# Optimization experiments

Hardware: AMD Instinct MI355X
Metric: run time of the kernel (lower is better)

## Reference

```python
import jax, jax.numpy as jnp
import numpy as np

PH, PW = 7, 7          # pooled_height, pooled_width
SCALE = 0.0625         # spatial_scale
K = 6                  # static max integer cells per bin side (max bin size = 448*SCALE/7 = 4)


def setup_inputs() -> dict:
    key = jax.random.key(0)
    kf, kb, kx, ky, kw, kh = jax.random.split(key, 6)
    B, C, H, W = 4, 256, 64, 64
    R = 1024
    features = jax.random.normal(kf, (B, C, H, W), dtype=jnp.float32)
    # rois rows: (batch_idx, x1, y1, x2, y2) in image coords (image ~1024px, scale 1/16)
    bidx = jax.random.randint(kb, (R,), 0, B).astype(jnp.float32)
    x1 = jax.random.uniform(kx, (R,), minval=0.0, maxval=576.0)
    y1 = jax.random.uniform(ky, (R,), minval=0.0, maxval=576.0)
    bw = jax.random.uniform(kw, (R,), minval=32.0, maxval=448.0)
    bh = jax.random.uniform(kh, (R,), minval=32.0, maxval=448.0)
    rois = jnp.stack([bidx, x1, y1, x1 + bw, y1 + bh], axis=1)
    return {"features": features, "rois": rois}


def _gather(features, b, hidx, widx, H, W):
    # hidx: [R,PH] int32, widx: [R,PW] int32 -> [R,PH,PW,C]; out-of-bounds reads are zero
    vh = (hidx >= 0) & (hidx < H)
    vw = (widx >= 0) & (widx < W)
    mask = (vh[:, :, None] & vw[:, None, :]).astype(features.dtype)  # [R,PH,PW]
    hc = jnp.clip(hidx, 0, H - 1)
    wc = jnp.clip(widx, 0, W - 1)
    d = features[b[:, None, None], :, hc[:, :, None], wc[:, None, :]]  # [R,PH,PW,C]
    return d * mask[..., None]


def _cell_weights(start, end, s):
    # exact integrals of the two 1D bilinear hat weights over [start,end] clipped to cell [s, s+1]
    y0 = jnp.maximum(start, s)
    yl = jnp.maximum(jnp.minimum(end, s + 1.0), y0)  # empty intersection -> zero weights
    a = y0 - s
    la = yl - s
    g0 = la - 0.5 * la * la - a + 0.5 * a * a  # weight of node at s
    g1 = 0.5 * la * la - 0.5 * a * a           # weight of node at s+1
    return g0, g1


def prroi_pool(features, rois):
    B, C, H, W = features.shape
    R = rois.shape[0]
    dt = features.dtype
    b = rois[:, 0].astype(jnp.int32)
    x1 = rois[:, 1] * SCALE
    y1 = rois[:, 2] * SCALE
    x2 = rois[:, 3] * SCALE
    y2 = rois[:, 4] * SCALE
    roi_w = jnp.maximum(x2 - x1, 0.0)
    roi_h = jnp.maximum(y2 - y1, 0.0)
    bin_w = roi_w / PW
    bin_h = roi_h / PH
    # per-bin continuous windows [ws, we)
    ws_w = x1[:, None] + bin_w[:, None] * jnp.arange(PW, dtype=dt)  # [R,PW]
    ws_h = y1[:, None] + bin_h[:, None] * jnp.arange(PH, dtype=dt)  # [R,PH]
    we_w = ws_w + bin_w[:, None]
    we_h = ws_h + bin_h[:, None]
    s0_w = jnp.floor(ws_w)
    s0_h = jnp.floor(ws_h)

    offs = np.stack(np.meshgrid(np.arange(K), np.arange(K), indexing="ij"), -1).reshape(-1, 2)
    offs = jnp.asarray(offs, dtype=dt)  # [K*K, 2] (dh, dw)

    def step(acc, off):
        sh = s0_h + off[0]  # [R,PH] float (integer-valued)
        sw = s0_w + off[1]  # [R,PW]
        gy0, gy1 = _cell_weights(ws_h, we_h, sh)
        gx0, gx1 = _cell_weights(ws_w, we_w, sw)
        hi = sh.astype(jnp.int32)
        wi = sw.astype(jnp.int32)
        d00 = _gather(features, b, hi, wi, H, W)
        d01 = _gather(features, b, hi, wi + 1, H, W)
        d10 = _gather(features, b, hi + 1, wi, H, W)
        d11 = _gather(features, b, hi + 1, wi + 1, H, W)
        gy0 = gy0[:, :, None, None]
        gy1 = gy1[:, :, None, None]
        gx0 = gx0[:, None, :, None]
        gx1 = gx1[:, None, :, None]
        contrib = d00 * (gy0 * gx0) + d01 * (gy0 * gx1) + d10 * (gy1 * gx0) + d11 * (gy1 * gx1)
        return acc + contrib, None

    acc0 = jnp.zeros((R, PH, PW, C), dtype=dt)
    acc, _ = jax.lax.scan(step, acc0, offs)
    win = (bin_w * bin_h)[:, None, None, None]  # bin area in feature coords
    out = jnp.where(win > 0, acc / jnp.where(win > 0, win, 1.0), 0.0)
    return jnp.transpose(out, (0, 3, 1, 2))  # [R, C, PH, PW]


def reference(features, rois):
    return prroi_pool(features, rois)
```

## Files before the change

### kernel.cpp

```cpp
#include <hip/hip_runtime.h>
#include <hip/hip_fp16.h>

#define R_    1024
#define B_    4
#define C_    256
#define H_    64
#define W_    64
#define HW_   4096
#define PHW_  49
#define ROIT  128
#define LROWF 258
#define SLACKH 16896

__device__ __forceinline__ void cell_w(float start, float end, float s, float& g0, float& g1) {
    float y0 = fmaxf(start, s);
    float yl = fmaxf(fminf(end, s + 1.0f), y0);
    float a  = y0 - s;
    float la = yl - s;
    g0 = la - 0.5f * la * la - a + 0.5f * a * a;
    g1 = 0.5f * la * la - 0.5f * a * a;
}

__device__ __forceinline__ float4 h4_to_f4(uint2 u) {
    __half2 a = *reinterpret_cast<__half2*>(&u.x);
    __half2 b = *reinterpret_cast<__half2*>(&u.y);
    float2 fa = __half22float2(a);
    float2 fb = __half22float2(b);
    return make_float4(fa.x, fa.y, fb.x, fb.y);
}

__global__ __launch_bounds__(256) void prep(const float* __restrict__ in,
                                            __half* __restrict__ fTh,
                                            const float* __restrict__ rois,
                                            int* __restrict__ perm,
                                            float* __restrict__ roitab) {
    int bid = blockIdx.x;
    if (bid < 4096) {
        __shared__ float tile[32][33];
        int b   = bid >> 10;
        int rem = bid & 1023;
        int c0  = (rem >> 7) * 32;
        int p0  = (rem & 127) * 32;
        int tx  = threadIdx.x & 31;
        int ty  = threadIdx.x >> 5;
        const float* src = in + (size_t)b * C_ * HW_;
#pragma unroll
        for (int i = 0; i < 32; i += 8)
            tile[ty + i][tx] = src[(size_t)(c0 + ty + i) * HW_ + (p0 + tx)];
        __syncthreads();
        __half2* dsth = (__half2*)(fTh + (size_t)b * HW_ * C_);
#pragma unroll
        for (int i = 0; i < 2; ++i) {
            int idx = threadIdx.x + i * 256;
            int py  = idx >> 4;
            int cp  = idx & 15;
            float lo = tile[cp * 2][py];
            float hi = tile[cp * 2 + 1][py];
            dsth[(size_t)(p0 + py) * (C_ / 2) + (c0 >> 1) + cp] = __floats2half2_rn(lo, hi);
        }
        return;
    }
    if (bid == 4096) {
        if (threadIdx.x >= 64) {
            for (int j = threadIdx.x - 64; j < SLACKH; j += 192)
                fTh[(size_t)B_ * HW_ * C_ + j] = __half(0.0f);
            return;
        }
        int lane = threadIdx.x;
        unsigned long long below = (1ull << lane) - 1ull;
        int key[16];
#pragma unroll
        for (int i = 0; i < 16; ++i) {
            int idx = i * 64 + lane;
            const float* roi = rois + idx * 5;
            int b = (int)roi[0];
            float yc = (roi[2] + roi[4]) * 0.5f * 0.0625f;
            int yb = min(3, max(0, (int)(yc * 0.0625f)));
            key[i] = b * 4 + yb;
        }
        int cntk[16];
#pragma unroll
        for (int k = 0; k < 16; ++k) cntk[k] = 0;
        for (int i = 0; i < 16; ++i)
#pragma unroll
            for (int k = 0; k < 16; ++k)
                cntk[k] += __popcll(__ballot(key[i] == k));
        int off[16]; int acc = 0;
#pragma unroll
        for (int k = 0; k < 16; ++k) { off[k] = acc; acc += cntk[k]; }
        for (int i = 0; i < 16; ++i) {
#pragma unroll
            for (int k = 0; k < 16; ++k) {
                unsigned long long m = __ballot(key[i] == k);
                if (key[i] == k)
                    perm[off[k] + __popcll(m & below)] = i * 64 + lane;
                off[k] += __popcll(m);
            }
        }
        return;
    }
    int i = (bid - 4097) * 256 + threadIdx.x;
    int r  = i / PHW_;
    int k  = i - r * PHW_;
    int ph = k / 7, pw = k - ph * 7;
    const float* roi = rois + r * 5;
    int bb = (int)roi[0];
    float x1 = roi[1] * 0.0625f, y1 = roi[2] * 0.0625f;
    float x2 = roi[3] * 0.0625f, y2 = roi[4] * 0.0625f;
    float rw = fmaxf(x2 - x1, 0.0f), rh = fmaxf(y2 - y1, 0.0f);
    float bw = rw / 7.0f, bh = rh / 7.0f;
    float win = bw * bh;
    float* rt = roitab + (size_t)r * ROIT;

    float wy[8], wx[7];
#pragma unroll
    for (int t = 0; t < 7; ++t) { wy[t] = 0.0f; wx[t] = 0.0f; }
    wy[7] = 0.0f;
    int w0 = 0, h0 = 0, npy = 0, w00 = 0;
    float invwin = 0.0f;
    if (win > 0.0f) {
        float ws = x1 + bw * (float)pw, we = ws + bw;
        float hs = y1 + bh * (float)ph, he = hs + bh;
        float s0w = floorf(ws), s0h = floorf(hs);
        w0 = (int)s0w; h0 = (int)s0h;
        w00 = (int)floorf(x1);
#pragma unroll
        for (int o = 0; o < 6; ++o) {
            float g0, g1;
            cell_w(hs, he, s0h + (float)o, g0, g1);
            wy[o] += g0; wy[o + 1] += g1;
            cell_w(ws, we, s0w + (float)o, g0, g1);
            wx[o] += g0; wx[o + 1] += g1;
        }
        npy = min(7, max(0, (int)ceilf(he - s0h + 1.0f)));
        int npx = min(7, max(0, (int)ceilf(we - s0w + 1.0f)));
        npy = max(0, min(npy, H_ - h0));
        npx = max(0, min(npx, W_ - w0));
#pragma unroll
        for (int t = 0; t < 7; ++t) {
            if (t >= npx) wx[t] = 0.0f;
            if (t >= npy) wy[t] = 0.0f;
        }
        invwin = 1.0f / win;
    }
    if (ph == 0) {
#pragma unroll
        for (int t = 0; t < 7; ++t) rt[pw * 7 + t] = wx[t];
        rt[49 + pw] = __int_as_float(w0 - w00);
    }
    if (pw == 0) {
#pragma unroll
        for (int t = 0; t < 8; ++t) rt[72 + ph * 8 + t] = wy[t] * invwin;
        rt[64 + ph] = __int_as_float(h0 | (npy << 8));
    }
    if (k == 0) {
        int jlim = 0;
        if (win > 0.0f) {
#pragma unroll
            for (int p = 0; p < 7; ++p) {
                float wsp = x1 + bw * (float)p, wep = wsp + bw;
                float s0wp = floorf(wsp);
                int w0p = (int)s0wp;
                int npxp = min(7, max(0, (int)ceilf(wep - s0wp + 1.0f)));
                npxp = max(0, min(npxp, W_ - w0p));
                jlim = max(jlim, (w0p - w00) + npxp);
            }
        }
        rt[63] = __int_as_float(bb | (w00 << 8) | (jlim << 16));
    }
}

__global__ __launch_bounds__(256) void prroi_rows(const __half* __restrict__ fTh,
                                                  const int* __restrict__ perm,
                                                  const float* __restrict__ roitab,
                                                  __half* __restrict__ scr) {
    __shared__ __align__(16) float colw[4][32 * 8];
    int wid  = __builtin_amdgcn_readfirstlane(threadIdx.x >> 6);
    int lane = threadIdx.x & 63;
    float* cwv = colw[wid];
    int bid = blockIdx.x;
    int g   = (bid & 7) * 896 + (bid >> 3) * 4 + wid;
    int rs  = g / 7;
    int ph  = g - rs * 7;
    int r   = __builtin_amdgcn_readfirstlane(perm[rs]);
    const float* rt = roitab + (size_t)r * ROIT;

#pragma unroll
    for (int u = 0; u < 4; ++u) cwv[lane + u * 64] = 0.0f;
    if (lane < 49) {
        int pw = lane / 7;
        int dx = lane - pw * 7;
        float wxv = rt[lane];
        int d = __float_as_int(rt[49 + pw]);
        cwv[(d + dx) * 8 + pw] = wxv;
    }
    int meta = __float_as_int(rt[63]);
    int bb   = meta & 0xff;
    int w00  = (meta >> 8) & 0xff;
    int jlim = (meta >> 16) & 0xff;
    int hm   = __float_as_int(rt[64 + ph]);
    int h0   = hm & 0xff;
    int npy  = (hm >> 8) & 0xff;
    int npy2 = (npy + 1) & ~1;
    const float* wyp = rt + 72 + ph * 8;
    const __half* fr = fTh + ((size_t)bb * HW_ + (size_t)h0 * W_ + w00) * C_ + lane * 4;

    float4 acc[7];
#pragma unroll
    for (int p = 0; p < 7; ++p) acc[p] = make_float4(0.f, 0.f, 0.f, 0.f);

    for (int jl = 0; jl < jlim; jl += 2) {
        const __half* cp = fr + (size_t)jl * C_;
        float4 gA = make_float4(0.f, 0.f, 0.f, 0.f);
        float4 gB = make_float4(0.f, 0.f, 0.f, 0.f);
        for (int dy = 0; dy < npy2; dy += 2) {
            const __half* r0 = cp + (size_t)dy * (W_ * C_);
            uint2 va0 = *(const uint2*)(r0);
            uint2 vb0 = *(const uint2*)(r0 + C_);
            uint2 va1 = *(const uint2*)(r0 + W_ * C_);
            uint2 vb1 = *(const uint2*)(r0 + W_ * C_ + C_);
            float w0y = wyp[dy];
            float w1y = wyp[dy + 1];
            float4 fa0 = h4_to_f4(va0);
            float4 fb0 = h4_to_f4(vb0);
            float4 fa1 = h4_to_f4(va1);
            float4 fb1 = h4_to_f4(vb1);
            gA.x = fmaf(w0y, fa0.x, fmaf(w1y, fa1.x, gA.x));
            gA.y = fmaf(w0y, fa0.y, fmaf(w1y, fa1.y, gA.y));
            gA.z = fmaf(w0y, fa0.z, fmaf(w1y, fa1.z, gA.z));
            gA.w = fmaf(w0y, fa0.w, fmaf(w1y, fa1.w, gA.w));
            gB.x = fmaf(w0y, fb0.x, fmaf(w1y, fb1.x, gB.x));
            gB.y = fmaf(w0y, fb0.y, fmaf(w1y, fb1.y, gB.y));
            gB.z = fmaf(w0y, fb0.z, fmaf(w1y, fb1.z, gB.z));
            gB.w = fmaf(w0y, fb0.w, fmaf(w1y, fb1.w, gB.w));
        }
        float4 ca0 = *(const float4*)(cwv + jl * 8);
        float4 ca1 = *(const float4*)(cwv + jl * 8 + 4);
        float4 cb0 = *(const float4*)(cwv + jl * 8 + 8);
        float4 cb1 = *(const float4*)(cwv + jl * 8 + 12);
#define ACCP(P, CA, CB) { \
    acc[P].x = fmaf(CA, gA.x, fmaf(CB, gB.x, acc[P].x)); \
    acc[P].y = fmaf(CA, gA.y, fmaf(CB, gB.y, acc[P].y)); \
    acc[P].z = fmaf(CA, gA.z, fmaf(CB, gB.z, acc[P].z)); \
    acc[P].w = fmaf(CA, gA.w, fmaf(CB, gB.w, acc[P].w)); }
        ACCP(0, ca0.x, cb0.x); ACCP(1, ca0.y, cb0.y); ACCP(2, ca0.z, cb0.z);
        ACCP(3, ca0.w, cb0.w); ACCP(4, ca1.x, cb1.x); ACCP(5, ca1.y, cb1.y);
        ACCP(6, ca1.z, cb1.z);
#undef ACCP
    }
    __half* sb = scr + ((size_t)r * PHW_ + ph * 7) * C_ + lane * 4;
#pragma unroll
    for (int p = 0; p < 7; ++p) {
        union { __half2 h2[2]; uint2 u; } pk2;
        pk2.h2[0] = __floats2half2_rn(acc[p].x, acc[p].y);
        pk2.h2[1] = __floats2half2_rn(acc[p].z, acc[p].w);
        *(uint2*)(sb + (size_t)p * C_) = pk2.u;
    }
}

__global__ __launch_bounds__(256) void fixup(const int* __restrict__ perm,
                                             const __half* __restrict__ scr,
                                             float* __restrict__ out) {
    __shared__ __align__(4) __half lds_h[PHW_ * LROWF];
    int bid  = blockIdx.x;
    int spos = ((bid & 7) << 7) | (bid >> 3);
    int r    = perm[spos];
    const unsigned int* src = (const unsigned int*)(scr + (size_t)r * PHW_ * C_);
    for (int j = threadIdx.x; j < PHW_ * (C_ / 2); j += 256) {
        int row = j >> 7;
        int col = j & 127;
        *(unsigned int*)&lds_h[row * LROWF + col * 2] = src[j];
    }
    __syncthreads();
    float* outr = out + (size_t)r * (C_ * PHW_);
#pragma unroll 4
    for (int j = threadIdx.x; j < C_ * PHW_; j += 256) {
        int c = j / PHW_;
        int k = j - c * PHW_;
        outr[j] = __half2float(lds_h[k * LROWF + c]);
    }
}

__global__ __launch_bounds__(256) void prroi_pool_direct(const float* __restrict__ f,
                                                         const float* __restrict__ rois,
                                                         float* __restrict__ out) {
    int bin = blockIdx.x;
    int r  = bin / PHW_;
    int k  = bin - r * PHW_;
    int ph = k / 7;
    int pw = k - ph * 7;
    int c = threadIdx.x;

    const float* roi = rois + r * 5;
    int bb = (int)roi[0];
    float x1 = roi[1] * 0.0625f, y1 = roi[2] * 0.0625f;
    float x2 = roi[3] * 0.0625f, y2 = roi[4] * 0.0625f;
    float rw = fmaxf(x2 - x1, 0.0f), rh = fmaxf(y2 - y1, 0.0f);
    float bw = rw / 7.0f, bh = rh / 7.0f;
    float win = bw * bh;
    size_t oidx = ((size_t)r * C_ + c) * PHW_ + k;
    if (!(win > 0.0f)) { out[oidx] = 0.0f; return; }

    float ws = x1 + bw * (float)pw, we = ws + bw;
    float hs = y1 + bh * (float)ph, he = hs + bh;
    float s0w = floorf(ws), s0h = floorf(hs);
    int w0 = (int)s0w, h0 = (int)s0h;
    float wy[7], wx[7];
#pragma unroll
    for (int t = 0; t < 7; ++t) { wy[t] = 0.0f; wx[t] = 0.0f; }
#pragma unroll
    for (int o = 0; o < 6; ++o) {
        float g0, g1;
        cell_w(hs, he, s0h + (float)o, g0, g1);
        wy[o] += g0; wy[o + 1] += g1;
        cell_w(ws, we, s0w + (float)o, g0, g1);
        wx[o] += g0; wx[o + 1] += g1;
    }
    int npy = min(7, max(0, (int)ceilf(he - s0h + 1.0f)));
    int npx = min(7, max(0, (int)ceilf(we - s0w + 1.0f)));
    npy = max(0, min(npy, H_ - h0));
    npx = max(0, min(npx, W_ - w0));

    const float* fbc = f + ((size_t)bb * C_ + c) * (H_ * W_);
    float acc = 0.0f;
#pragma unroll
    for (int dy = 0; dy < 7; ++dy) {
        if (dy < npy) {
            float row = 0.0f;
#pragma unroll
            for (int dx = 0; dx < 7; ++dx) {
                if (dx < npx)
                    row = fmaf(wx[dx], fbc[(h0 + dy) * W_ + (w0 + dx)], row);
            }
            acc = fmaf(wy[dy], row, acc);
        }
    }
    out[oidx] = acc / win;
}

extern "C" void kernel_launch(void* const* d_in, const int* in_sizes, int n_in,
                              void* d_out, int out_size, void* d_ws, size_t ws_size,
                              hipStream_t stream) {
    const float* feat = (const float*)d_in[0];
    const float* rois = (const float*)d_in[1];
    float* out = (float*)d_out;

    const size_t fth_b   = (size_t)B_ * HW_ * C_ * sizeof(__half);
    const size_t slack_b = (size_t)SLACKH * sizeof(__half);
    const size_t perm_b  = (size_t)R_ * sizeof(int);
    const size_t rt_b    = (size_t)R_ * ROIT * sizeof(float);
    const size_t scr_b   = (size_t)R_ * PHW_ * C_ * sizeof(__half);

    if (ws_size >= fth_b + slack_b + perm_b + rt_b + scr_b) {
        __half* fTh  = (__half*)d_ws;
        int*    perm = (int*)((char*)d_ws + fth_b + slack_b);
        float*  rtab = (float*)((char*)d_ws + fth_b + slack_b + perm_b);
        __half* scr  = (__half*)((char*)d_ws + fth_b + slack_b + perm_b + rt_b);
        prep<<<4293, 256, 0, stream>>>(feat, fTh, rois, perm, rtab);
        prroi_rows<<<1792, 256, 0, stream>>>(fTh, perm, rtab, scr);
        fixup<<<R_, 256, 0, stream>>>(perm, scr, out);
    } else {
        prroi_pool_direct<<<R_ * PHW_, 256, 0, stream>>>(feat, rois, out);
    }
}
```

Baseline: 68.32 us.

## Precompute per-ROI column coefficient table and use separable row-then-column accumulation

Adds 1024 extra prep blocks that build a per-ROI table of combined column weights (g0 of a cell plus g1 of the previous cell) for each output column. A new rows kernel first reduces the feature rows vertically with the row weights for each column pair, then spreads the result to the seven pooled outputs using the precomputed coefficients, with no LDS staging. This drops the shared-memory column-weight setup and reuses each vertically reduced column across all output bins, at the cost of an extra 1 MB table, a larger slack region, and seven float4 accumulators per thread. The old LDS path is kept as a fallback for smaller workspaces.

```diff
diff --git a/kernel.cpp b/kernel.cpp
--- a/kernel.cpp
+++ b/kernel.cpp
@@ -10,7 +10,7 @@
 #define PHW_  49
 #define ROIT  128
 #define LROWF 258
-#define SLACKH 16896
+#define SLACKH 17408
 
 __device__ __forceinline__ void cell_w(float start, float end, float s, float& g0, float& g1) {
     float y0 = fmaxf(start, s);
@@ -33,7 +33,8 @@
                                             __half* __restrict__ fTh,
                                             const float* __restrict__ rois,
                                             int* __restrict__ perm,
-                                            float* __restrict__ roitab) {
+                                            float* __restrict__ roitab,
+                                            float* __restrict__ ctab) {
     int bid = blockIdx.x;
     if (bid < 4096) {
         __shared__ float tile[32][33];
@@ -97,6 +98,35 @@
                 off[k] += __popcll(m);
             }
         }
+        return;
+    }
+    if (bid >= 4293) {
+        int r   = bid - 4293;
+        int tid = threadIdx.x;
+        int jl  = tid >> 3;
+        int p   = tid & 7;
+        const float* roi = rois + r * 5;
+        float x1 = roi[1] * 0.0625f, y1 = roi[2] * 0.0625f;
+        float x2 = roi[3] * 0.0625f, y2 = roi[4] * 0.0625f;
+        float rw = fmaxf(x2 - x1, 0.0f), rh = fmaxf(y2 - y1, 0.0f);
+        float bw = rw / 7.0f, bh = rh / 7.0f;
+        float coef = 0.0f;
+        if (bw * bh > 0.0f && p < 7) {
+            float ws = x1 + bw * (float)p, we = ws + bw;
+            float s0w = floorf(ws);
+            int w0p = (int)s0w;
+            int w00 = (int)floorf(x1);
+            int dx  = jl - (w0p - w00);
+            int npx = min(7, max(0, (int)ceilf(we - s0w + 1.0f)));
+            npx = max(0, min(npx, W_ - w0p));
+            if (dx >= 0 && dx < npx) {
+                float g0a, g1a, g0b, g1b;
+                cell_w(ws, we, s0w + (float)dx, g0a, g1a);
+                cell_w(ws, we, s0w + (float)(dx - 1), g0b, g1b);
+                coef = g0a + g1b;
+            }
+        }
+        ctab[((size_t)r << 8) + tid] = coef;
         return;
     }
     int i = (bid - 4097) * 256 + threadIdx.x;
@@ -170,10 +200,89 @@
     }
 }
 
-__global__ __launch_bounds__(256) void prroi_rows(const __half* __restrict__ fTh,
-                                                  const int* __restrict__ perm,
-                                                  const float* __restrict__ roitab,
-                                                  __half* __restrict__ scr) {
+__global__ __launch_bounds__(256, 8) void prroi_rows_ct(const __half* __restrict__ fTh,
+                                                        const int* __restrict__ perm,
+                                                        const float* __restrict__ roitab,
+                                                        const float* __restrict__ ctab,
+                                                        __half* __restrict__ scr) {
+    int wid  = __builtin_amdgcn_readfirstlane(threadIdx.x >> 6);
+    int lane = threadIdx.x & 63;
+    int bid  = blockIdx.x;
+    int g    = (bid & 7) * 896 + (bid >> 3) * 4 + wid;
+    int rs   = g / 7;
+    int ph   = g - rs * 7;
+    int r    = __builtin_amdgcn_readfirstlane(perm[rs]);
+    const float* rt = roitab + (size_t)r * ROIT;
+    const float* ct = ctab + ((size_t)r << 8);
+
+    int meta = __float_as_int(rt[63]);
+    int bb   = meta & 0xff;
+    int w00  = (meta >> 8) & 0xff;
+    int jlim = (meta >> 16) & 0xff;
+    int hm   = __float_as_int(rt[64 + ph]);
+    int h0   = hm & 0xff;
+    int npy  = (hm >> 8) & 0xff;
+    int npy2 = (npy + 1) & ~1;
+    const float* wyp = rt + 72 + ph * 8;
+    const __half* fr = fTh + ((size_t)bb * HW_ + (size_t)h0 * W_ + w00) * C_ + lane * 4;
+
+    float4 acc[7];
+#pragma unroll
+    for (int p = 0; p < 7; ++p) acc[p] = make_float4(0.f, 0.f, 0.f, 0.f);
+
+    for (int jl = 0; jl < jlim; jl += 2) {
+        float4 ca0 = *(const float4*)(ct + jl * 8);
+        float4 ca1 = *(const float4*)(ct + jl * 8 + 4);
+        float4 cb0 = *(const float4*)(ct + jl * 8 + 8);
+        float4 cb1 = *(const float4*)(ct + jl * 8 + 12);
+        const __half* cp = fr + (size_t)jl * C_;
+        float4 gA = make_float4(0.f, 0.f, 0.f, 0.f);
+        float4 gB = make_float4(0.f, 0.f, 0.f, 0.f);
+        for (int dy = 0; dy < npy2; dy += 2) {
+            const __half* r0 = cp + (size_t)dy * (W_ * C_);
+            uint2 va0 = *(const uint2*)(r0);
+            uint2 vb0 = *(const uint2*)(r0 + C_);
+            uint2 va1 = *(const uint2*)(r0 + W_ * C_);
+            uint2 vb1 = *(const uint2*)(r0 + W_ * C_ + C_);
+            float w0y = wyp[dy];
+            float w1y = wyp[dy + 1];
+            float4 fa0 = h4_to_f4(va0);
+            float4 fb0 = h4_to_f4(vb0);
+            float4 fa1 = h4_to_f4(va1);
+            float4 fb1 = h4_to_f4(vb1);
+            gA.x = fmaf(w0y, fa0.x, fmaf(w1y, fa1.x, gA.x));
+            gA.y = fmaf(w0y, fa0.y, fmaf(w1y, fa1.y, gA.y));
+            gA.z = fmaf(w0y, fa0.z, fmaf(w1y, fa1.z, gA.z));
+            gA.w = fmaf(w0y, fa0.w, fmaf(w1y, fa1.w, gA.w));
+            gB.x = fmaf(w0y, fb0.x, fmaf(w1y, fb1.x, gB.x));
+            gB.y = fmaf(w0y, fb0.y, fmaf(w1y, fb1.y, gB.y));
+            gB.z = fmaf(w0y, fb0.z, fmaf(w1y, fb1.z, gB.z));
+            gB.w = fmaf(w0y, fb0.w, fmaf(w1y, fb1.w, gB.w));
+        }
+#define ACCP(P, CA, CB) { \
+    acc[P].x = fmaf(CA, gA.x, fmaf(CB, gB.x, acc[P].x)); \
+    acc[P].y = fmaf(CA, gA.y, fmaf(CB, gB.y, acc[P].y)); \
+    acc[P].z = fmaf(CA, gA.z, fmaf(CB, gB.z, acc[P].z)); \
+    acc[P].w = fmaf(CA, gA.w, fmaf(CB, gB.w, acc[P].w)); }
+        ACCP(0, ca0.x, cb0.x); ACCP(1, ca0.y, cb0.y); ACCP(2, ca0.z, cb0.z);
+        ACCP(3, ca0.w, cb0.w); ACCP(4, ca1.x, cb1.x); ACCP(5, ca1.y, cb1.y);
+        ACCP(6, ca1.z, cb1.z);
+#undef ACCP
+    }
+    __half* sb = scr + ((size_t)r * PHW_ + ph * 7) * C_ + lane * 4;
+#pragma unroll
+    for (int p = 0; p < 7; ++p) {
+        union { __half2 h2[2]; uint2 u; } pk2;
+        pk2.h2[0] = __floats2half2_rn(acc[p].x, acc[p].y);
+        pk2.h2[1] = __floats2half2_rn(acc[p].z, acc[p].w);
+        *(uint2*)(sb + (size_t)p * C_) = pk2.u;
+    }
+}
+
+__global__ __launch_bounds__(256) void prroi_rows_lds(const __half* __restrict__ fTh,
+                                                      const int* __restrict__ perm,
+                                                      const float* __restrict__ roitab,
+                                                      __half* __restrict__ scr) {
     __shared__ __align__(16) float colw[4][32 * 8];
     int wid  = __builtin_amdgcn_readfirstlane(threadIdx.x >> 6);
     int lane = threadIdx.x & 63;
@@ -349,15 +458,26 @@
     const size_t slack_b = (size_t)SLACKH * sizeof(__half);
     const size_t perm_b  = (size_t)R_ * sizeof(int);
     const size_t rt_b    = (size_t)R_ * ROIT * sizeof(float);
+    const size_t ct_b    = (size_t)R_ * 256 * sizeof(float);
     const size_t scr_b   = (size_t)R_ * PHW_ * C_ * sizeof(__half);
 
-    if (ws_size >= fth_b + slack_b + perm_b + rt_b + scr_b) {
+    const size_t base = fth_b + slack_b + perm_b + rt_b;
+    if (ws_size >= base + ct_b + scr_b) {
         __half* fTh  = (__half*)d_ws;
         int*    perm = (int*)((char*)d_ws + fth_b + slack_b);
         float*  rtab = (float*)((char*)d_ws + fth_b + slack_b + perm_b);
-        __half* scr  = (__half*)((char*)d_ws + fth_b + slack_b + perm_b + rt_b);
-        prep<<<4293, 256, 0, stream>>>(feat, fTh, rois, perm, rtab);
-        prroi_rows<<<1792, 256, 0, stream>>>(fTh, perm, rtab, scr);
+        float*  ctab = (float*)((char*)d_ws + base);
+        __half* scr  = (__half*)((char*)d_ws + base + ct_b);
+        prep<<<5317, 256, 0, stream>>>(feat, fTh, rois, perm, rtab, ctab);
+        prroi_rows_ct<<<1792, 256, 0, stream>>>(fTh, perm, rtab, ctab, scr);
+        fixup<<<R_, 256, 0, stream>>>(perm, scr, out);
+    } else if (ws_size >= base + scr_b) {
+        __half* fTh  = (__half*)d_ws;
+        int*    perm = (int*)((char*)d_ws + fth_b + slack_b);
+        float*  rtab = (float*)((char*)d_ws + fth_b + slack_b + perm_b);
+        __half* scr  = (__half*)((char*)d_ws + base);
+        prep<<<4293, 256, 0, stream>>>(feat, fTh, rois, perm, rtab, (float*)nullptr);
+        prroi_rows_lds<<<1792, 256, 0, stream>>>(fTh, perm, rtab, scr);
         fixup<<<R_, 256, 0, stream>>>(perm, scr, out);
     } else {
         prroi_pool_direct<<<R_ * PHW_, 256, 0, stream>>>(feat, rois, out);
```

Result: no change. 68.49 us (+0.2%).
